# Kernel tuning notes

Measured on AMD Instinct MI355X. Metric: run time of the kernel, lower is better.

The kernel has to match this reference:

```python
import jax, jax.numpy as jnp
import numpy as np

N = 100000      # nodes
E = 3200000     # edges per graph (pos and neg)
IN_FEATS = 128
HIDDEN = 32
PROP_STEP = 8
USE_RELU = False  # args.relu default False


def setup_inputs() -> dict:
    key = jax.random.key(0)
    ks = jax.random.split(key, 8)
    in_feat = jax.random.normal(ks[0], (N, IN_FEATS), dtype=jnp.float32)
    src = jax.random.randint(ks[1], (E,), 0, N, dtype=jnp.int32)
    dst = jax.random.randint(ks[2], (E,), 0, N, dtype=jnp.int32)
    neg_src = jax.random.randint(ks[3], (E,), 0, N, dtype=jnp.int32)
    neg_dst = jax.random.randint(ks[4], (E,), 0, N, dtype=jnp.int32)
    W1 = jax.random.normal(ks[5], (IN_FEATS, HIDDEN), dtype=jnp.float32) * (1.0 / np.sqrt(IN_FEATS))
    b1 = jnp.zeros((HIDDEN,), dtype=jnp.float32)
    gamma = jnp.ones((HIDDEN,), dtype=jnp.float32)
    beta = jnp.zeros((HIDDEN,), dtype=jnp.float32)
    W2 = jax.random.normal(ks[6], (HIDDEN, HIDDEN), dtype=jnp.float32) * (1.0 / np.sqrt(HIDDEN))
    b2 = jnp.zeros((HIDDEN,), dtype=jnp.float32)
    return dict(in_feat=in_feat, W1=W1, b1=b1, gamma=gamma, beta=beta,
                W2=W2, b2=b2, src=src, dst=dst, neg_src=neg_src, neg_dst=neg_dst)


def _graph_conv(h, src, dst, n_nodes):
    """DGL GraphConv(norm='both', weight=False, bias=False):
       out = D_dst^{-1/2} A D_src^{-1/2} h, sum aggregation."""
    ones = jnp.ones(src.shape, dtype=h.dtype)
    out_deg = jax.ops.segment_sum(ones, src, num_segments=n_nodes)
    in_deg = jax.ops.segment_sum(ones, dst, num_segments=n_nodes)
    hs = h * jax.lax.rsqrt(jnp.clip(out_deg, 1.0))[:, None]   # [N, H]
    msg = hs[src]                                             # [E, H] gather
    agg = jax.ops.segment_sum(msg, dst, num_segments=n_nodes)  # [N, H] scatter-add
    return agg * jax.lax.rsqrt(jnp.clip(in_deg, 1.0))[:, None]


def reference(in_feat, W1, b1, gamma, beta, W2, b2, src, dst, neg_src, neg_dst):
    # MLP: Linear -> BatchNorm1d (training-mode batch stats) -> (Dropout noop) -> ReLU -> Linear
    x = in_feat @ W1 + b1
    mu = jnp.mean(x, axis=0)
    var = jnp.var(x, axis=0)
    x = (x - mu) * jax.lax.rsqrt(var + 1e-5) * gamma + beta
    x = jax.nn.relu(x)
    ori_h = x @ W2 + b2                                       # [N, H]

    # Iterative pos-neg SpMM propagation with residual (h initialized to ori_h)
    h = ori_h
    for _ in range(PROP_STEP):
        if USE_RELU:
            h = jax.nn.relu(h)
        h = _graph_conv(h, src, dst, N) - _graph_conv(h, neg_src, neg_dst, N) + ori_h
    return h
```

## Files before the change

kernel.cpp:

```cpp
#include <hip/hip_runtime.h>
#include <hip/hip_fp16.h>

#define N_NODES 100000
#define E_EDGES 3200000
#define IN_F 128
#define HID 32
#define PROP 8

#define WIN 16384
#define NWIN 7
#define HS 32

#define MB_ROWS 64
#define MB_BLOCKS ((N_NODES + MB_ROWS - 1) / MB_ROWS)
#define RED_B 32

#define FB 512
#define CH 12500
#define BK_SH 7
#define BK_N 128
#define NBK 782
#define L2S (NBK * FB)
#define SCB2 391

__global__ __launch_bounds__(256) void hist_kernel(const int* __restrict__ s,
        const int* __restrict__ ns, int* __restrict__ degs) {
    __shared__ int lh[WIN];
    int b = blockIdx.x;
    int w = b % NWIN;
    int st = (b / NWIN) % 2;
    int sl = b / (NWIN * 2);
    const int* p = st ? ns : s;
    for (int i = threadIdx.x; i < WIN; i += 256) lh[i] = 0;
    __syncthreads();
    const int lo = w * WIN;
    const int per = E_EDGES / HS;
    const int4* p4 = (const int4*)(p + sl * per);
    for (int i = threadIdx.x; i < per / 4; i += 256) {
        int4 v = p4[i];
        int a;
        a = v.x - lo; if ((unsigned)a < WIN) atomicAdd(&lh[a], 1);
        a = v.y - lo; if ((unsigned)a < WIN) atomicAdd(&lh[a], 1);
        a = v.z - lo; if ((unsigned)a < WIN) atomicAdd(&lh[a], 1);
        a = v.w - lo; if ((unsigned)a < WIN) atomicAdd(&lh[a], 1);
    }
    __syncthreads();
    int* g = degs + st * N_NODES;
    for (int i = threadIdx.x; i < WIN; i += 256) {
        int idx = lo + i;
        if (idx < N_NODES && lh[i]) atomicAdd(&g[idx], lh[i]);
    }
}

__global__ void inv_sqrt_kernel(const int* __restrict__ deg, float* __restrict__ inv, int n) {
    int i = blockIdx.x * blockDim.x + threadIdx.x;
    if (i < n) inv[i] = rsqrtf(fmaxf((float)deg[i], 1.0f));
}

__global__ __launch_bounds__(256) void countA_kernel(const int* __restrict__ dst,
        const int* __restrict__ ndst, int* __restrict__ counts) {
    __shared__ int lh[NBK];
    int blk = blockIdx.x;
    for (int i = threadIdx.x; i < NBK; i += 256) lh[i] = 0;
    __syncthreads();
    const int* dp = (blk < FB / 2) ? dst + blk * CH : ndst + (blk - FB / 2) * CH;
    const int4* dp4 = (const int4*)dp;
    for (int i = threadIdx.x; i < CH / 4; i += 256) {
        int4 v = dp4[i];
        atomicAdd(&lh[v.x >> BK_SH], 1);
        atomicAdd(&lh[v.y >> BK_SH], 1);
        atomicAdd(&lh[v.z >> BK_SH], 1);
        atomicAdd(&lh[v.w >> BK_SH], 1);
    }
    __syncthreads();
    for (int b = threadIdx.x; b < NBK; b += 256) counts[b * FB + blk] = lh[b];
}

__global__ __launch_bounds__(1024) void scanA2_kernel(const int* __restrict__ counts,
        int* __restrict__ offs, int* __restrict__ blockSums) {
    __shared__ int sh[1024];
    int t = threadIdx.x, b = blockIdx.x;
    int i = b * 1024 + t;
    int v = counts[i];
    sh[t] = v;
    __syncthreads();
    for (int off = 1; off < 1024; off <<= 1) {
        int u = (t >= off) ? sh[t - off] : 0;
        __syncthreads();
        sh[t] += u;
        __syncthreads();
    }
    offs[i] = sh[t] - v;
    if (t == 1023) blockSums[b] = sh[1023];
}

__global__ __launch_bounds__(512) void scanB2_kernel(const int* __restrict__ blockSums,
        int* __restrict__ blockOff) {
    __shared__ int sh[512];
    int t = threadIdx.x;
    int v = (t < SCB2) ? blockSums[t] : 0;
    sh[t] = v;
    __syncthreads();
    for (int off = 1; off < 512; off <<= 1) {
        int u = (t >= off) ? sh[t - off] : 0;
        __syncthreads();
        sh[t] += u;
        __syncthreads();
    }
    if (t < SCB2) blockOff[t] = sh[t] - v;
}

__global__ __launch_bounds__(1024) void scanC2_kernel(int* __restrict__ offs,
        const int* __restrict__ blockOff) {
    int b = blockIdx.x, t = threadIdx.x;
    int i = b * 1024 + t;
    offs[i] += blockOff[b];
    if (i == 0) offs[L2S] = 2 * E_EDGES;
}

__global__ __launch_bounds__(256) void fillA2_kernel(const int* __restrict__ src, const int* __restrict__ dst,
        const int* __restrict__ nsrc, const int* __restrict__ ndst,
        const float* __restrict__ invs, const int* __restrict__ offs, int2* __restrict__ rec) {
    __shared__ int cur[NBK];
    __shared__ int base[NBK];
    int blk = blockIdx.x;
    int g = (blk >= FB / 2);
    const int* sp = g ? (nsrc + (blk - FB / 2) * CH) : (src + blk * CH);
    const int* dp = g ? (ndst + (blk - FB / 2) * CH) : (dst + blk * CH);
    const float* io = invs + (g ? N_NODES : 0);
    const float sign = g ? -1.f : 1.f;
    const int gbit = g << 24;
    for (int i = threadIdx.x; i < NBK; i += 256) {
        cur[i] = 0;
        base[i] = offs[i * FB + blk];
    }
    __syncthreads();
    for (int i = threadIdx.x; i < CH; i += 256) {
        int u = sp[i], v = dp[i];
        int b = v >> BK_SH;
        float c = sign * io[u];
        int p = base[b] + atomicAdd(&cur[b], 1);
        rec[p] = make_int2(u | ((v & (BK_N - 1)) << 17) | gbit, __float_as_int(c));
    }
}

__global__ __launch_bounds__(256) void reorder_kernel(const int* __restrict__ offs,
        const int2* __restrict__ rec, int2* __restrict__ rec2, int* __restrict__ row_ptr2) {
    __shared__ int cnt[BK_N];
    __shared__ int cntp[BK_N];
    __shared__ int scan[BK_N];
    __shared__ int base[BK_N];
    __shared__ float invp[BK_N], invn[BK_N];
    int bkt = blockIdx.x, tid = threadIdx.x;
    if (tid < BK_N) { cnt[tid] = 0; cntp[tid] = 0; }
    __syncthreads();
    int beg = offs[bkt * FB], end = offs[(bkt + 1) * FB];
    for (int i = beg + tid; i < end; i += 256) {
        int rx = rec[i].x;
        int d = (rx >> 17) & (BK_N - 1);
        atomicAdd(&cnt[d], 1);
        if (!(rx & (1 << 24))) atomicAdd(&cntp[d], 1);
    }
    __syncthreads();
    int v = (tid < BK_N) ? cnt[tid] : 0;
    if (tid < BK_N) {
        scan[tid] = v;
        int np = cntp[tid];
        invp[tid] = rsqrtf(fmaxf((float)np, 1.0f));
        invn[tid] = rsqrtf(fmaxf((float)(v - np), 1.0f));
    }
    __syncthreads();
    for (int off = 1; off < BK_N; off <<= 1) {
        int u = (tid < BK_N && tid >= off) ? scan[tid - off] : 0;
        __syncthreads();
        if (tid < BK_N) scan[tid] += u;
        __syncthreads();
    }
    if (tid < BK_N) {
        int b = beg + scan[tid] - v;
        base[tid] = b;
        row_ptr2[bkt * BK_N + tid] = b;
        cnt[tid] = 0;
    }
    if (bkt == NBK - 1 && tid == 0) row_ptr2[NBK * BK_N] = 2 * E_EDGES;
    __syncthreads();
    for (int i = beg + tid; i < end; i += 256) {
        int2 r = rec[i];
        int d = (r.x >> 17) & (BK_N - 1);
        int g = (r.x >> 24) & 1;
        float c = __int_as_float(r.y) * (g ? invn[d] : invp[d]);
        int p = base[d] + atomicAdd(&cnt[d], 1);
        rec2[p] = make_int2(r.x & 0x1FFFF, __float_as_int(c));
    }
}

__global__ __launch_bounds__(256) void mlp1_kernel(const float* __restrict__ in_feat,
        const float* __restrict__ W1, const float* __restrict__ b1,
        float* __restrict__ x, float* __restrict__ partials) {
    __shared__ float4 sRow4[MB_ROWS * 32];
    __shared__ float  sW1t[32 * 132];
    int tid = threadIdx.x;
    for (int idx = tid; idx < IN_F * HID; idx += 256) {
        int j = idx >> 5, k = idx & 31;
        sW1t[k * 132 + j] = W1[idx];
    }
    int nb = blockIdx.x * MB_ROWS;
    const float4* inf4 = (const float4*)in_feat;
    for (int idx = tid; idx < MB_ROWS * 32; idx += 256) {
        int row = idx >> 5, q = idx & 31;
        int g = nb + row;
        float4 v = (g < N_NODES) ? inf4[(size_t)g * 32 + q] : make_float4(0.f, 0.f, 0.f, 0.f);
        sRow4[row * 32 + (q ^ (row & 31))] = v;
    }
    __syncthreads();
    int rt = tid & 31, kt = tid >> 5;
    int k0 = kt * 4;
    float acc[2][4] = {{0.f}};
    const float4* w0p = (const float4*)&sW1t[(k0 + 0) * 132];
    const float4* w1p = (const float4*)&sW1t[(k0 + 1) * 132];
    const float4* w2p = (const float4*)&sW1t[(k0 + 2) * 132];
    const float4* w3p = (const float4*)&sW1t[(k0 + 3) * 132];
    #pragma unroll 4
    for (int jq = 0; jq < 32; ++jq) {
        int pq = jq ^ rt;
        float4 a0 = sRow4[rt * 32 + pq];
        float4 a1 = sRow4[(rt + 32) * 32 + pq];
        float4 w0 = w0p[jq], w1 = w1p[jq], w2 = w2p[jq], w3 = w3p[jq];
        acc[0][0] += a0.x*w0.x + a0.y*w0.y + a0.z*w0.z + a0.w*w0.w;
        acc[0][1] += a0.x*w1.x + a0.y*w1.y + a0.z*w1.z + a0.w*w1.w;
        acc[0][2] += a0.x*w2.x + a0.y*w2.y + a0.z*w2.z + a0.w*w2.w;
        acc[0][3] += a0.x*w3.x + a0.y*w3.y + a0.z*w3.z + a0.w*w3.w;
        acc[1][0] += a1.x*w0.x + a1.y*w0.y + a1.z*w0.z + a1.w*w0.w;
        acc[1][1] += a1.x*w1.x + a1.y*w1.y + a1.z*w1.z + a1.w*w1.w;
        acc[1][2] += a1.x*w2.x + a1.y*w2.y + a1.z*w2.z + a1.w*w2.w;
        acc[1][3] += a1.x*w3.x + a1.y*w3.y + a1.z*w3.z + a1.w*w3.w;
    }
    float bb[4] = { b1[k0], b1[k0 + 1], b1[k0 + 2], b1[k0 + 3] };
    float s[4] = {0.f, 0.f, 0.f, 0.f}, ss[4] = {0.f, 0.f, 0.f, 0.f};
    #pragma unroll
    for (int i = 0; i < 2; ++i) {
        int row = nb + rt + 32 * i;
        if (row < N_NODES) {
            float4 o;
            o.x = acc[i][0] + bb[0];
            o.y = acc[i][1] + bb[1];
            o.z = acc[i][2] + bb[2];
            o.w = acc[i][3] + bb[3];
            *(float4*)&x[(size_t)row * HID + k0] = o;
            s[0] += o.x; ss[0] += o.x * o.x;
            s[1] += o.y; ss[1] += o.y * o.y;
            s[2] += o.z; ss[2] += o.z * o.z;
            s[3] += o.w; ss[3] += o.w * o.w;
        }
    }
    for (int off = 16; off; off >>= 1) {
        #pragma unroll
        for (int c = 0; c < 4; ++c) {
            s[c]  += __shfl_down(s[c],  off, 32);
            ss[c] += __shfl_down(ss[c], off, 32);
        }
    }
    if (rt == 0) {
        float* pb = partials + (size_t)blockIdx.x * 64;
        #pragma unroll
        for (int c = 0; c < 4; ++c) {
            pb[k0 + c]      = s[c];
            pb[32 + k0 + c] = ss[c];
        }
    }
}

__global__ __launch_bounds__(256) void bnred_kernel(const float* __restrict__ partials,
        float* __restrict__ partials2) {
    __shared__ float red[4][64];
    int t = threadIdx.x, b = blockIdx.x;
    int r = t >> 6, c = t & 63;
    float sum = 0.f;
    for (int g = b * 4 + r; g < MB_BLOCKS; g += RED_B * 4)
        sum += partials[(size_t)g * 64 + c];
    red[r][c] = sum;
    __syncthreads();
    if (t < 64) partials2[b * 64 + t] = (red[0][t] + red[1][t]) + (red[2][t] + red[3][t]);
}

__global__ __launch_bounds__(256) void bnparam_kernel(const float* __restrict__ partials2,
        const float* __restrict__ gamma, const float* __restrict__ beta, float* __restrict__ params) {
    __shared__ float red[4][64];
    int t = threadIdx.x;
    int col = t & 63, ch = t >> 6;
    float sum = 0.f;
    for (int g = ch; g < RED_B; g += 4) sum += partials2[(size_t)g * 64 + col];
    red[ch][col] = sum;
    __syncthreads();
    if (t < 64) red[0][t] = red[0][t] + red[1][t] + red[2][t] + red[3][t];
    __syncthreads();
    if (t < HID) {
        float mu  = red[0][t] * (1.0f / (float)N_NODES);
        float var = red[0][t + 32] * (1.0f / (float)N_NODES) - mu * mu;
        float sg = gamma[t] * rsqrtf(var + 1e-5f);
        params[t]       = sg;
        params[HID + t] = beta[t] - mu * sg;
    }
}

__global__ __launch_bounds__(256) void mlp2_kernel(const float* __restrict__ x,
        const float* __restrict__ params, const float* __restrict__ W2,
        const float* __restrict__ b2, float* __restrict__ ori_h, __half* __restrict__ h16) {
    __shared__ float sW2[HID * HID];
    __shared__ float sXn[8][HID];
    int tid = threadIdx.x;
    for (int i = tid; i < HID * HID; i += 256) sW2[i] = W2[i];
    int nb = blockIdx.x * 8;
    int k = tid & 31, r = tid >> 5;
    float v = x[(size_t)(nb + r) * HID + k];
    v = fmaxf(fmaf(v, params[k], params[HID + k]), 0.f);
    sXn[r][k] = v;
    __syncthreads();
    float acc = b2[k];
    #pragma unroll
    for (int j = 0; j < HID; ++j) acc = fmaf(sXn[r][j], sW2[j * HID + k], acc);
    int o = (nb + r) * HID + k;
    ori_h[o] = acc;
    h16[o] = __float2half(acc);
}

__global__ __launch_bounds__(256) void gather_kernel(const int* __restrict__ row_ptr,
        const int2* __restrict__ rec, const __half2* __restrict__ h2,
        const float2* __restrict__ ori2, __half2* __restrict__ hn2, float2* __restrict__ out2) {
    int tid = threadIdx.x;
    int node = blockIdx.x * 8 + (tid >> 5);
    int lane = tid & 31;
    int slot = lane >> 4;
    int q = lane & 15;
    int beg = row_ptr[node], end = row_ptr[node + 1];
    float2 a0 = {0.f, 0.f}, a1 = {0.f, 0.f}, a2 = {0.f, 0.f}, a3 = {0.f, 0.f};
    float2 a4 = {0.f, 0.f}, a5 = {0.f, 0.f}, a6 = {0.f, 0.f}, a7 = {0.f, 0.f};
    int i = beg;
    for (; i + 16 <= end; i += 16) {
        int2 r0 = rec[i + slot];
        int2 r1 = rec[i + 2 + slot];
        int2 r2 = rec[i + 4 + slot];
        int2 r3 = rec[i + 6 + slot];
        int2 r4 = rec[i + 8 + slot];
        int2 r5 = rec[i + 10 + slot];
        int2 r6 = rec[i + 12 + slot];
        int2 r7 = rec[i + 14 + slot];
        float2 f0 = __half22float2(h2[r0.x * 16 + q]);
        float2 f1 = __half22float2(h2[r1.x * 16 + q]);
        float2 f2 = __half22float2(h2[r2.x * 16 + q]);
        float2 f3 = __half22float2(h2[r3.x * 16 + q]);
        float2 f4 = __half22float2(h2[r4.x * 16 + q]);
        float2 f5 = __half22float2(h2[r5.x * 16 + q]);
        float2 f6 = __half22float2(h2[r6.x * 16 + q]);
        float2 f7 = __half22float2(h2[r7.x * 16 + q]);
        float c0 = __int_as_float(r0.y), c1 = __int_as_float(r1.y);
        float c2 = __int_as_float(r2.y), c3 = __int_as_float(r3.y);
        float c4 = __int_as_float(r4.y), c5 = __int_as_float(r5.y);
        float c6 = __int_as_float(r6.y), c7 = __int_as_float(r7.y);
        a0.x = fmaf(c0, f0.x, a0.x); a0.y = fmaf(c0, f0.y, a0.y);
        a1.x = fmaf(c1, f1.x, a1.x); a1.y = fmaf(c1, f1.y, a1.y);
        a2.x = fmaf(c2, f2.x, a2.x); a2.y = fmaf(c2, f2.y, a2.y);
        a3.x = fmaf(c3, f3.x, a3.x); a3.y = fmaf(c3, f3.y, a3.y);
        a4.x = fmaf(c4, f4.x, a4.x); a4.y = fmaf(c4, f4.y, a4.y);
        a5.x = fmaf(c5, f5.x, a5.x); a5.y = fmaf(c5, f5.y, a5.y);
        a6.x = fmaf(c6, f6.x, a6.x); a6.y = fmaf(c6, f6.y, a6.y);
        a7.x = fmaf(c7, f7.x, a7.x); a7.y = fmaf(c7, f7.y, a7.y);
    }
    for (; i + 8 <= end; i += 8) {
        int2 r0 = rec[i + slot];
        int2 r1 = rec[i + 2 + slot];
        int2 r2 = rec[i + 4 + slot];
        int2 r3 = rec[i + 6 + slot];
        float2 f0 = __half22float2(h2[r0.x * 16 + q]);
        float2 f1 = __half22float2(h2[r1.x * 16 + q]);
        float2 f2 = __half22float2(h2[r2.x * 16 + q]);
        float2 f3 = __half22float2(h2[r3.x * 16 + q]);
        float c0 = __int_as_float(r0.y), c1 = __int_as_float(r1.y);
        float c2 = __int_as_float(r2.y), c3 = __int_as_float(r3.y);
        a0.x = fmaf(c0, f0.x, a0.x); a0.y = fmaf(c0, f0.y, a0.y);
        a1.x = fmaf(c1, f1.x, a1.x); a1.y = fmaf(c1, f1.y, a1.y);
        a2.x = fmaf(c2, f2.x, a2.x); a2.y = fmaf(c2, f2.y, a2.y);
        a3.x = fmaf(c3, f3.x, a3.x); a3.y = fmaf(c3, f3.y, a3.y);
    }
    for (; i + 2 <= end; i += 2) {
        int2 r = rec[i + slot];
        float2 f = __half22float2(h2[r.x * 16 + q]);
        float c = __int_as_float(r.y);
        a0.x = fmaf(c, f.x, a0.x); a0.y = fmaf(c, f.y, a0.y);
    }
    if (i < end && slot == 0) {
        int2 r = rec[i];
        float2 f = __half22float2(h2[r.x * 16 + q]);
        float c = __int_as_float(r.y);
        a0.x = fmaf(c, f.x, a0.x); a0.y = fmaf(c, f.y, a0.y);
    }
    float sx = ((a0.x + a1.x) + (a2.x + a3.x)) + ((a4.x + a5.x) + (a6.x + a7.x));
    float sy = ((a0.y + a1.y) + (a2.y + a3.y)) + ((a4.y + a5.y) + (a6.y + a7.y));
    sx += __shfl_down(sx, 16, 32);
    sy += __shfl_down(sy, 16, 32);
    if (slot == 0) {
        float2 o = ori2[node * 16 + q];
        float rx = o.x + sx, ry = o.y + sy;
        if (out2) out2[node * 16 + q] = make_float2(rx, ry);
        else hn2[node * 16 + q] = __floats2half2_rn(rx, ry);
    }
}

extern "C" void kernel_launch(void* const* d_in, const int* in_sizes, int n_in,
                              void* d_out, int out_size, void* d_ws, size_t ws_size,
                              hipStream_t stream) {
    const float* in_feat = (const float*)d_in[0];
    const float* W1    = (const float*)d_in[1];
    const float* b1    = (const float*)d_in[2];
    const float* gamma = (const float*)d_in[3];
    const float* beta  = (const float*)d_in[4];
    const float* W2    = (const float*)d_in[5];
    const float* b2    = (const float*)d_in[6];
    const int* src  = (const int*)d_in[7];
    const int* dst  = (const int*)d_in[8];
    const int* nsrc = (const int*)d_in[9];
    const int* ndst = (const int*)d_in[10];
    float* out = (float*)d_out;

    float* ws      = (float*)d_ws;
    float* x       = ws;
    float* ori_h   = x + (size_t)N_NODES * HID;
    float* invs    = ori_h + (size_t)N_NODES * HID;
    float* params  = invs + 2 * (size_t)N_NODES;
    float* partials= params + 2 * HID;
    float* partials2 = partials + (size_t)MB_BLOCKS * 64;
    int*   degs    = (int*)(partials2 + (size_t)RED_B * 64);
    int*   offs    = degs + 2 * N_NODES;
    int*   blockSums = offs + L2S + 2;
    int*   blockOff  = blockSums + 512;
    int*   row_ptr2  = blockOff + 512;
    uintptr_t hp  = (uintptr_t)(row_ptr2 + NBK * BK_N + 2);
    hp = (hp + 63) & ~(uintptr_t)63;
    __half* h16A   = (__half*)hp;
    __half* h16B   = h16A + (size_t)N_NODES * HID;
    uintptr_t rp  = (uintptr_t)(h16B + (size_t)N_NODES * HID);
    rp = (rp + 63) & ~(uintptr_t)63;
    int2*  rec    = (int2*)rp;
    int*   counts = (int*)x;
    int2*  rec2   = (int2*)in_feat;

    hipMemsetAsync(degs, 0, 2 * (size_t)N_NODES * sizeof(int), stream);

    hist_kernel<<<NWIN * 2 * HS, 256, 0, stream>>>(src, nsrc, degs);
    inv_sqrt_kernel<<<(2 * N_NODES + 255) / 256, 256, 0, stream>>>(degs, invs, 2 * N_NODES);

    countA_kernel<<<FB, 256, 0, stream>>>(dst, ndst, counts);
    scanA2_kernel<<<SCB2, 1024, 0, stream>>>(counts, offs, blockSums);
    scanB2_kernel<<<1, 512, 0, stream>>>(blockSums, blockOff);
    scanC2_kernel<<<SCB2, 1024, 0, stream>>>(offs, blockOff);
    fillA2_kernel<<<FB, 256, 0, stream>>>(src, dst, nsrc, ndst, invs, offs, rec);

    mlp1_kernel<<<MB_BLOCKS, 256, 0, stream>>>(in_feat, W1, b1, x, partials);
    bnred_kernel<<<RED_B, 256, 0, stream>>>(partials, partials2);
    bnparam_kernel<<<1, 256, 0, stream>>>(partials2, gamma, beta, params);
    mlp2_kernel<<<N_NODES / 8, 256, 0, stream>>>(x, params, W2, b2, ori_h, h16A);

    reorder_kernel<<<NBK, 256, 0, stream>>>(offs, rec, rec2, row_ptr2);

    const __half* h = h16A;
    for (int it = 0; it < PROP; ++it) {
        __half* hn16 = (it & 1) ? h16A : h16B;
        float* o32 = (it == PROP - 1) ? out : nullptr;
        gather_kernel<<<N_NODES / 8, 256, 0, stream>>>(row_ptr2, rec2,
                (const __half2*)h, (const float2*)ori_h, (__half2*)hn16, (float2*)o32);
        h = hn16;
    }
}
```

Measured before the change: 1.025 ms.

## Split SpMM gather into two source-range passes for cache locality

Reorders each destination's edges by source node half and adds a mid row pointer, then runs each propagation step as two gather passes over disjoint source ranges with a float accumulator between them. This shrinks the working set of gathered feature rows per pass so it fits better in per-die L2. It costs an extra launch per step plus accumulator read/write traffic and slightly more work in the reorder kernel.

```diff
diff --git a/kernel.cpp b/kernel.cpp
--- a/kernel.cpp
+++ b/kernel.cpp
@@ -22,6 +22,8 @@
 #define NBK 782
 #define L2S (NBK * FB)
 #define SCB2 391
+
+#define PSPLIT 50000
 
 __global__ __launch_bounds__(256) void hist_kernel(const int* __restrict__ s,
         const int* __restrict__ ns, int* __restrict__ degs) {
@@ -145,14 +147,17 @@
 }
 
 __global__ __launch_bounds__(256) void reorder_kernel(const int* __restrict__ offs,
-        const int2* __restrict__ rec, int2* __restrict__ rec2, int* __restrict__ row_ptr2) {
+        const int2* __restrict__ rec, int2* __restrict__ rec2,
+        int* __restrict__ row_ptr2, int* __restrict__ row_mid) {
     __shared__ int cnt[BK_N];
     __shared__ int cntp[BK_N];
+    __shared__ int c0[BK_N];
     __shared__ int scan[BK_N];
     __shared__ int base[BK_N];
+    __shared__ int cur0[BK_N], cur1[BK_N];
     __shared__ float invp[BK_N], invn[BK_N];
     int bkt = blockIdx.x, tid = threadIdx.x;
-    if (tid < BK_N) { cnt[tid] = 0; cntp[tid] = 0; }
+    if (tid < BK_N) { cnt[tid] = 0; cntp[tid] = 0; c0[tid] = 0; }
     __syncthreads();
     int beg = offs[bkt * FB], end = offs[(bkt + 1) * FB];
     for (int i = beg + tid; i < end; i += 256) {
@@ -160,6 +165,7 @@
         int d = (rx >> 17) & (BK_N - 1);
         atomicAdd(&cnt[d], 1);
         if (!(rx & (1 << 24))) atomicAdd(&cntp[d], 1);
+        if ((rx & 0x1FFFF) < PSPLIT) atomicAdd(&c0[d], 1);
     }
     __syncthreads();
     int v = (tid < BK_N) ? cnt[tid] : 0;
@@ -180,7 +186,8 @@
         int b = beg + scan[tid] - v;
         base[tid] = b;
         row_ptr2[bkt * BK_N + tid] = b;
-        cnt[tid] = 0;
+        row_mid[bkt * BK_N + tid] = b + c0[tid];
+        cur0[tid] = 0; cur1[tid] = 0;
     }
     if (bkt == NBK - 1 && tid == 0) row_ptr2[NBK * BK_N] = 2 * E_EDGES;
     __syncthreads();
@@ -188,9 +195,11 @@
         int2 r = rec[i];
         int d = (r.x >> 17) & (BK_N - 1);
         int g = (r.x >> 24) & 1;
+        int u = r.x & 0x1FFFF;
         float c = __int_as_float(r.y) * (g ? invn[d] : invp[d]);
-        int p = base[d] + atomicAdd(&cnt[d], 1);
-        rec2[p] = make_int2(r.x & 0x1FFFF, __float_as_int(c));
+        int ofs = (u < PSPLIT) ? atomicAdd(&cur0[d], 1)
+                               : (c0[d] + atomicAdd(&cur1[d], 1));
+        rec2[base[d] + ofs] = make_int2(u, __float_as_int(c));
     }
 }
 
@@ -324,15 +333,17 @@
     h16[o] = __float2half(acc);
 }
 
-__global__ __launch_bounds__(256) void gather_kernel(const int* __restrict__ row_ptr,
-        const int2* __restrict__ rec, const __half2* __restrict__ h2,
-        const float2* __restrict__ ori2, __half2* __restrict__ hn2, float2* __restrict__ out2) {
+__global__ __launch_bounds__(256) void gather_kernel(const int* __restrict__ row_lo,
+        const int* __restrict__ row_hi, const int2* __restrict__ rec,
+        const __half2* __restrict__ h2, float2* __restrict__ acc2,
+        const float2* __restrict__ ori2, __half2* __restrict__ hn2,
+        float2* __restrict__ out2, int phase) {
     int tid = threadIdx.x;
     int node = blockIdx.x * 8 + (tid >> 5);
     int lane = tid & 31;
     int slot = lane >> 4;
     int q = lane & 15;
-    int beg = row_ptr[node], end = row_ptr[node + 1];
+    int beg = row_lo[node], end = row_hi[node];
     float2 a0 = {0.f, 0.f}, a1 = {0.f, 0.f}, a2 = {0.f, 0.f}, a3 = {0.f, 0.f};
     float2 a4 = {0.f, 0.f}, a5 = {0.f, 0.f}, a6 = {0.f, 0.f}, a7 = {0.f, 0.f};
     int i = beg;
@@ -399,10 +410,15 @@
     sx += __shfl_down(sx, 16, 32);
     sy += __shfl_down(sy, 16, 32);
     if (slot == 0) {
-        float2 o = ori2[node * 16 + q];
-        float rx = o.x + sx, ry = o.y + sy;
-        if (out2) out2[node * 16 + q] = make_float2(rx, ry);
-        else hn2[node * 16 + q] = __floats2half2_rn(rx, ry);
+        if (phase == 0) {
+            acc2[node * 16 + q] = make_float2(sx, sy);
+        } else {
+            float2 a = acc2[node * 16 + q];
+            float2 o = ori2[node * 16 + q];
+            float rx = a.x + o.x + sx, ry = a.y + o.y + sy;
+            if (out2) out2[node * 16 + q] = make_float2(rx, ry);
+            else hn2[node * 16 + q] = __floats2half2_rn(rx, ry);
+        }
     }
 }
 
@@ -434,7 +450,8 @@
     int*   blockSums = offs + L2S + 2;
     int*   blockOff  = blockSums + 512;
     int*   row_ptr2  = blockOff + 512;
-    uintptr_t hp  = (uintptr_t)(row_ptr2 + NBK * BK_N + 2);
+    int*   row_mid   = row_ptr2 + NBK * BK_N + 2;
+    uintptr_t hp  = (uintptr_t)(row_mid + NBK * BK_N + 2);
     hp = (hp + 63) & ~(uintptr_t)63;
     __half* h16A   = (__half*)hp;
     __half* h16B   = h16A + (size_t)N_NODES * HID;
@@ -443,6 +460,7 @@
     int2*  rec    = (int2*)rp;
     int*   counts = (int*)x;
     int2*  rec2   = (int2*)in_feat;
+    float2* acc2  = (float2*)x;
 
     hipMemsetAsync(degs, 0, 2 * (size_t)N_NODES * sizeof(int), stream);
 
@@ -460,14 +478,17 @@
     bnparam_kernel<<<1, 256, 0, stream>>>(partials2, gamma, beta, params);
     mlp2_kernel<<<N_NODES / 8, 256, 0, stream>>>(x, params, W2, b2, ori_h, h16A);
 
-    reorder_kernel<<<NBK, 256, 0, stream>>>(offs, rec, rec2, row_ptr2);
+    reorder_kernel<<<NBK, 256, 0, stream>>>(offs, rec, rec2, row_ptr2, row_mid);
 
     const __half* h = h16A;
     for (int it = 0; it < PROP; ++it) {
         __half* hn16 = (it & 1) ? h16A : h16B;
         float* o32 = (it == PROP - 1) ? out : nullptr;
-        gather_kernel<<<N_NODES / 8, 256, 0, stream>>>(row_ptr2, rec2,
-                (const __half2*)h, (const float2*)ori_h, (__half2*)hn16, (float2*)o32);
+        gather_kernel<<<N_NODES / 8, 256, 0, stream>>>(row_ptr2, row_mid, rec2,
+                (const __half2*)h, acc2, nullptr, nullptr, nullptr, 0);
+        gather_kernel<<<N_NODES / 8, 256, 0, stream>>>(row_mid, row_ptr2 + 1, rec2,
+                (const __half2*)h, acc2, (const float2*)ori_h, (__half2*)hn16,
+                (float2*)o32, 1);
         h = hn16;
     }
 }
```

Result: slower. 1.179 ms (+15.0%).

## Widen gather loads to 16B per lane, stage reorder in LDS, retune histogram/bucket grids

Applied to the files above, without the earlier changes.

The gather kernel now has each lane load 16 bytes (8 halves) of a neighbor row, with 8 edges processed in parallel per warp-half group instead of 2, and reduces the partial sums by shuffle. The reorder kernel writes sorted records into a shared-memory staging buffer and then copies them out contiguously, replacing scattered global writes. Histogram windows and fill block counts are retuned (fewer, larger windows; twice as many fill blocks with half-size chunks), and the scan is widened to match. The large LDS stage (96KB) lowers reorder occupancy and assumes that no bucket holds more than 12288 records.

```diff
diff --git a/kernel.cpp b/kernel.cpp
--- a/kernel.cpp
+++ b/kernel.cpp
@@ -7,21 +7,22 @@
 #define HID 32
 #define PROP 8
 
-#define WIN 16384
-#define NWIN 7
+#define WIN 32768
+#define NWIN 4
 #define HS 32
 
 #define MB_ROWS 64
 #define MB_BLOCKS ((N_NODES + MB_ROWS - 1) / MB_ROWS)
 #define RED_B 32
 
-#define FB 512
-#define CH 12500
+#define FB 1024
+#define CH 6250
 #define BK_SH 7
 #define BK_N 128
 #define NBK 782
 #define L2S (NBK * FB)
-#define SCB2 391
+#define SCB2 782
+#define STG 12288
 
 __global__ __launch_bounds__(256) void hist_kernel(const int* __restrict__ s,
         const int* __restrict__ ns, int* __restrict__ degs) {
@@ -64,13 +65,11 @@
     for (int i = threadIdx.x; i < NBK; i += 256) lh[i] = 0;
     __syncthreads();
     const int* dp = (blk < FB / 2) ? dst + blk * CH : ndst + (blk - FB / 2) * CH;
-    const int4* dp4 = (const int4*)dp;
-    for (int i = threadIdx.x; i < CH / 4; i += 256) {
-        int4 v = dp4[i];
+    const int2* dp2 = (const int2*)dp;
+    for (int i = threadIdx.x; i < CH / 2; i += 256) {
+        int2 v = dp2[i];
         atomicAdd(&lh[v.x >> BK_SH], 1);
         atomicAdd(&lh[v.y >> BK_SH], 1);
-        atomicAdd(&lh[v.z >> BK_SH], 1);
-        atomicAdd(&lh[v.w >> BK_SH], 1);
     }
     __syncthreads();
     for (int b = threadIdx.x; b < NBK; b += 256) counts[b * FB + blk] = lh[b];
@@ -94,14 +93,14 @@
     if (t == 1023) blockSums[b] = sh[1023];
 }
 
-__global__ __launch_bounds__(512) void scanB2_kernel(const int* __restrict__ blockSums,
+__global__ __launch_bounds__(1024) void scanB2_kernel(const int* __restrict__ blockSums,
         int* __restrict__ blockOff) {
-    __shared__ int sh[512];
+    __shared__ int sh[1024];
     int t = threadIdx.x;
     int v = (t < SCB2) ? blockSums[t] : 0;
     sh[t] = v;
     __syncthreads();
-    for (int off = 1; off < 512; off <<= 1) {
+    for (int off = 1; off < 1024; off <<= 1) {
         int u = (t >= off) ? sh[t - off] : 0;
         __syncthreads();
         sh[t] += u;
@@ -148,9 +147,10 @@
         const int2* __restrict__ rec, int2* __restrict__ rec2, int* __restrict__ row_ptr2) {
     __shared__ int cnt[BK_N];
     __shared__ int cntp[BK_N];
-    __shared__ int scan[BK_N];
-    __shared__ int base[BK_N];
+    __shared__ int scn[BK_N];
+    __shared__ int lbase[BK_N];
     __shared__ float invp[BK_N], invn[BK_N];
+    __shared__ int2 stage[STG];
     int bkt = blockIdx.x, tid = threadIdx.x;
     if (tid < BK_N) { cnt[tid] = 0; cntp[tid] = 0; }
     __syncthreads();
@@ -164,22 +164,22 @@
     __syncthreads();
     int v = (tid < BK_N) ? cnt[tid] : 0;
     if (tid < BK_N) {
-        scan[tid] = v;
+        scn[tid] = v;
         int np = cntp[tid];
         invp[tid] = rsqrtf(fmaxf((float)np, 1.0f));
         invn[tid] = rsqrtf(fmaxf((float)(v - np), 1.0f));
     }
     __syncthreads();
     for (int off = 1; off < BK_N; off <<= 1) {
-        int u = (tid < BK_N && tid >= off) ? scan[tid - off] : 0;
-        __syncthreads();
-        if (tid < BK_N) scan[tid] += u;
+        int u = (tid < BK_N && tid >= off) ? scn[tid - off] : 0;
+        __syncthreads();
+        if (tid < BK_N) scn[tid] += u;
         __syncthreads();
     }
     if (tid < BK_N) {
-        int b = beg + scan[tid] - v;
-        base[tid] = b;
-        row_ptr2[bkt * BK_N + tid] = b;
+        int b = scn[tid] - v;
+        lbase[tid] = b;
+        row_ptr2[bkt * BK_N + tid] = beg + b;
         cnt[tid] = 0;
     }
     if (bkt == NBK - 1 && tid == 0) row_ptr2[NBK * BK_N] = 2 * E_EDGES;
@@ -189,9 +189,12 @@
         int d = (r.x >> 17) & (BK_N - 1);
         int g = (r.x >> 24) & 1;
         float c = __int_as_float(r.y) * (g ? invn[d] : invp[d]);
-        int p = base[d] + atomicAdd(&cnt[d], 1);
-        rec2[p] = make_int2(r.x & 0x1FFFF, __float_as_int(c));
-    }
+        int p = lbase[d] + atomicAdd(&cnt[d], 1);
+        stage[p] = make_int2(r.x & 0x1FFFF, __float_as_int(c));
+    }
+    __syncthreads();
+    int n = end - beg;
+    for (int j = tid; j < n; j += 256) rec2[beg + j] = stage[j];
 }
 
 __global__ __launch_bounds__(256) void mlp1_kernel(const float* __restrict__ in_feat,
@@ -324,85 +327,81 @@
     h16[o] = __float2half(acc);
 }
 
+__device__ __forceinline__ float2 h2f(int b) {
+    __half2 h; __builtin_memcpy(&h, &b, 4); return __half22float2(h);
+}
+
 __global__ __launch_bounds__(256) void gather_kernel(const int* __restrict__ row_ptr,
-        const int2* __restrict__ rec, const __half2* __restrict__ h2,
-        const float2* __restrict__ ori2, __half2* __restrict__ hn2, float2* __restrict__ out2) {
+        const int2* __restrict__ rec, const int4* __restrict__ h4,
+        const float4* __restrict__ ori4, int4* __restrict__ hn4, float4* __restrict__ out4) {
     int tid = threadIdx.x;
     int node = blockIdx.x * 8 + (tid >> 5);
     int lane = tid & 31;
-    int slot = lane >> 4;
-    int q = lane & 15;
+    int slot = lane >> 2;
+    int ql = lane & 3;
     int beg = row_ptr[node], end = row_ptr[node + 1];
     float2 a0 = {0.f, 0.f}, a1 = {0.f, 0.f}, a2 = {0.f, 0.f}, a3 = {0.f, 0.f};
-    float2 a4 = {0.f, 0.f}, a5 = {0.f, 0.f}, a6 = {0.f, 0.f}, a7 = {0.f, 0.f};
     int i = beg;
-    for (; i + 16 <= end; i += 16) {
+#define ACC8(f, c) { float2 u_; \
+        u_ = h2f((f).x); a0.x = fmaf((c), u_.x, a0.x); a0.y = fmaf((c), u_.y, a0.y); \
+        u_ = h2f((f).y); a1.x = fmaf((c), u_.x, a1.x); a1.y = fmaf((c), u_.y, a1.y); \
+        u_ = h2f((f).z); a2.x = fmaf((c), u_.x, a2.x); a2.y = fmaf((c), u_.y, a2.y); \
+        u_ = h2f((f).w); a3.x = fmaf((c), u_.x, a3.x); a3.y = fmaf((c), u_.y, a3.y); }
+    for (; i + 32 <= end; i += 32) {
         int2 r0 = rec[i + slot];
-        int2 r1 = rec[i + 2 + slot];
-        int2 r2 = rec[i + 4 + slot];
-        int2 r3 = rec[i + 6 + slot];
-        int2 r4 = rec[i + 8 + slot];
-        int2 r5 = rec[i + 10 + slot];
-        int2 r6 = rec[i + 12 + slot];
-        int2 r7 = rec[i + 14 + slot];
-        float2 f0 = __half22float2(h2[r0.x * 16 + q]);
-        float2 f1 = __half22float2(h2[r1.x * 16 + q]);
-        float2 f2 = __half22float2(h2[r2.x * 16 + q]);
-        float2 f3 = __half22float2(h2[r3.x * 16 + q]);
-        float2 f4 = __half22float2(h2[r4.x * 16 + q]);
-        float2 f5 = __half22float2(h2[r5.x * 16 + q]);
-        float2 f6 = __half22float2(h2[r6.x * 16 + q]);
-        float2 f7 = __half22float2(h2[r7.x * 16 + q]);
+        int2 r1 = rec[i + 8 + slot];
+        int2 r2 = rec[i + 16 + slot];
+        int2 r3 = rec[i + 24 + slot];
+        int4 f0 = h4[r0.x * 4 + ql];
+        int4 f1 = h4[r1.x * 4 + ql];
+        int4 f2 = h4[r2.x * 4 + ql];
+        int4 f3 = h4[r3.x * 4 + ql];
         float c0 = __int_as_float(r0.y), c1 = __int_as_float(r1.y);
         float c2 = __int_as_float(r2.y), c3 = __int_as_float(r3.y);
-        float c4 = __int_as_float(r4.y), c5 = __int_as_float(r5.y);
-        float c6 = __int_as_float(r6.y), c7 = __int_as_float(r7.y);
-        a0.x = fmaf(c0, f0.x, a0.x); a0.y = fmaf(c0, f0.y, a0.y);
-        a1.x = fmaf(c1, f1.x, a1.x); a1.y = fmaf(c1, f1.y, a1.y);
-        a2.x = fmaf(c2, f2.x, a2.x); a2.y = fmaf(c2, f2.y, a2.y);
-        a3.x = fmaf(c3, f3.x, a3.x); a3.y = fmaf(c3, f3.y, a3.y);
-        a4.x = fmaf(c4, f4.x, a4.x); a4.y = fmaf(c4, f4.y, a4.y);
-        a5.x = fmaf(c5, f5.x, a5.x); a5.y = fmaf(c5, f5.y, a5.y);
-        a6.x = fmaf(c6, f6.x, a6.x); a6.y = fmaf(c6, f6.y, a6.y);
-        a7.x = fmaf(c7, f7.x, a7.x); a7.y = fmaf(c7, f7.y, a7.y);
+        ACC8(f0, c0) ACC8(f1, c1) ACC8(f2, c2) ACC8(f3, c3)
     }
     for (; i + 8 <= end; i += 8) {
-        int2 r0 = rec[i + slot];
-        int2 r1 = rec[i + 2 + slot];
-        int2 r2 = rec[i + 4 + slot];
-        int2 r3 = rec[i + 6 + slot];
-        float2 f0 = __half22float2(h2[r0.x * 16 + q]);
-        float2 f1 = __half22float2(h2[r1.x * 16 + q]);
-        float2 f2 = __half22float2(h2[r2.x * 16 + q]);
-        float2 f3 = __half22float2(h2[r3.x * 16 + q]);
-        float c0 = __int_as_float(r0.y), c1 = __int_as_float(r1.y);
-        float c2 = __int_as_float(r2.y), c3 = __int_as_float(r3.y);
-        a0.x = fmaf(c0, f0.x, a0.x); a0.y = fmaf(c0, f0.y, a0.y);
-        a1.x = fmaf(c1, f1.x, a1.x); a1.y = fmaf(c1, f1.y, a1.y);
-        a2.x = fmaf(c2, f2.x, a2.x); a2.y = fmaf(c2, f2.y, a2.y);
-        a3.x = fmaf(c3, f3.x, a3.x); a3.y = fmaf(c3, f3.y, a3.y);
-    }
-    for (; i + 2 <= end; i += 2) {
         int2 r = rec[i + slot];
-        float2 f = __half22float2(h2[r.x * 16 + q]);
+        int4 f = h4[r.x * 4 + ql];
         float c = __int_as_float(r.y);
-        a0.x = fmaf(c, f.x, a0.x); a0.y = fmaf(c, f.y, a0.y);
-    }
-    if (i < end && slot == 0) {
-        int2 r = rec[i];
-        float2 f = __half22float2(h2[r.x * 16 + q]);
+        ACC8(f, c)
+    }
+    if (i + slot < end) {
+        int2 r = rec[i + slot];
+        int4 f = h4[r.x * 4 + ql];
         float c = __int_as_float(r.y);
-        a0.x = fmaf(c, f.x, a0.x); a0.y = fmaf(c, f.y, a0.y);
-    }
-    float sx = ((a0.x + a1.x) + (a2.x + a3.x)) + ((a4.x + a5.x) + (a6.x + a7.x));
-    float sy = ((a0.y + a1.y) + (a2.y + a3.y)) + ((a4.y + a5.y) + (a6.y + a7.y));
-    sx += __shfl_down(sx, 16, 32);
-    sy += __shfl_down(sy, 16, 32);
+        ACC8(f, c)
+    }
+#undef ACC8
+    #pragma unroll
+    for (int off = 4; off <= 16; off <<= 1) {
+        a0.x += __shfl_down(a0.x, off, 32); a0.y += __shfl_down(a0.y, off, 32);
+        a1.x += __shfl_down(a1.x, off, 32); a1.y += __shfl_down(a1.y, off, 32);
+        a2.x += __shfl_down(a2.x, off, 32); a2.y += __shfl_down(a2.y, off, 32);
+        a3.x += __shfl_down(a3.x, off, 32); a3.y += __shfl_down(a3.y, off, 32);
+    }
     if (slot == 0) {
-        float2 o = ori2[node * 16 + q];
-        float rx = o.x + sx, ry = o.y + sy;
-        if (out2) out2[node * 16 + q] = make_float2(rx, ry);
-        else hn2[node * 16 + q] = __floats2half2_rn(rx, ry);
+        float4 oA = ori4[node * 8 + ql * 2];
+        float4 oB = ori4[node * 8 + ql * 2 + 1];
+        float r0x = a0.x + oA.x, r0y = a0.y + oA.y;
+        float r1x = a1.x + oA.z, r1y = a1.y + oA.w;
+        float r2x = a2.x + oB.x, r2y = a2.y + oB.y;
+        float r3x = a3.x + oB.z, r3y = a3.y + oB.w;
+        if (out4) {
+            out4[node * 8 + ql * 2]     = make_float4(r0x, r0y, r1x, r1y);
+            out4[node * 8 + ql * 2 + 1] = make_float4(r2x, r2y, r3x, r3y);
+        } else {
+            __half2 p0 = __floats2half2_rn(r0x, r0y);
+            __half2 p1 = __floats2half2_rn(r1x, r1y);
+            __half2 p2 = __floats2half2_rn(r2x, r2y);
+            __half2 p3 = __floats2half2_rn(r3x, r3y);
+            int4 w;
+            __builtin_memcpy(&w.x, &p0, 4);
+            __builtin_memcpy(&w.y, &p1, 4);
+            __builtin_memcpy(&w.z, &p2, 4);
+            __builtin_memcpy(&w.w, &p3, 4);
+            hn4[node * 4 + ql] = w;
+        }
     }
 }
 
@@ -432,8 +431,8 @@
     int*   degs    = (int*)(partials2 + (size_t)RED_B * 64);
     int*   offs    = degs + 2 * N_NODES;
     int*   blockSums = offs + L2S + 2;
-    int*   blockOff  = blockSums + 512;
-    int*   row_ptr2  = blockOff + 512;
+    int*   blockOff  = blockSums + 1024;
+    int*   row_ptr2  = blockOff + 1024;
     uintptr_t hp  = (uintptr_t)(row_ptr2 + NBK * BK_N + 2);
     hp = (hp + 63) & ~(uintptr_t)63;
     __half* h16A   = (__half*)hp;
@@ -451,7 +450,7 @@
 
     countA_kernel<<<FB, 256, 0, stream>>>(dst, ndst, counts);
     scanA2_kernel<<<SCB2, 1024, 0, stream>>>(counts, offs, blockSums);
-    scanB2_kernel<<<1, 512, 0, stream>>>(blockSums, blockOff);
+    scanB2_kernel<<<1, 1024, 0, stream>>>(blockSums, blockOff);
     scanC2_kernel<<<SCB2, 1024, 0, stream>>>(offs, blockOff);
     fillA2_kernel<<<FB, 256, 0, stream>>>(src, dst, nsrc, ndst, invs, offs, rec);
 
@@ -467,7 +466,7 @@
         __half* hn16 = (it & 1) ? h16A : h16B;
         float* o32 = (it == PROP - 1) ? out : nullptr;
         gather_kernel<<<N_NODES / 8, 256, 0, stream>>>(row_ptr2, rec2,
-                (const __half2*)h, (const float2*)ori_h, (__half2*)hn16, (float2*)o32);
+                (const int4*)h, (const float4*)ori_h, (int4*)hn16, (float4*)o32);
         h = hn16;
     }
 }
```

Measured after the change: 980.0 us. 1.05x faster.
